# Optimization experiments

Hardware: AMD Instinct MI355X
Metric: run time of the kernel (lower is better)

The kernel has to match this reference:

```python
import jax, jax.numpy as jnp
import numpy as np

K = 1024      # num_embeddings
D = 256       # embedding_dim
BETA = 0.25


def setup_inputs() -> dict:
    key = jax.random.key(0)
    k1, k2 = jax.random.split(key)
    z = jax.random.normal(k1, (4, D, 16, 32, 32), dtype=jnp.float32)
    # matches torch init: uniform(-1/K, 1/K)
    embedding = jax.random.uniform(k2, (K, D), dtype=jnp.float32,
                                   minval=-1.0 / K, maxval=1.0 / K)
    return {"z": z, "embedding": embedding}


def reference(z, embedding):
    # z: (B, C, Dd, H, W) with C == D
    z_perm = jnp.transpose(z, (0, 2, 3, 4, 1))          # (B, Dd, H, W, C)
    flat = z_perm.reshape(-1, D)                        # (N, D)

    dist = (jnp.sum(flat * flat, axis=1, keepdims=True)
            + jnp.sum(embedding * embedding, axis=1)
            - 2.0 * flat @ embedding.T)
    indices_flat = jnp.argmin(dist, axis=1)             # (N,)

    # one-hot @ embedding == direct gather
    z_q_flat = embedding[indices_flat]                  # (N, D)
    z_q = z_q_flat.reshape(z_perm.shape)

    commitment_loss = jnp.mean((z_perm - jax.lax.stop_gradient(z_q)) ** 2)
    vq_loss = BETA * commitment_loss

    # straight-through estimator
    z_q_st = z_perm + jax.lax.stop_gradient(z_q - z_perm)
    z_q_out = jnp.transpose(z_q_st, (0, 4, 1, 2, 3))    # back to (B, C, Dd, H, W)

    # perplexity from assignment histogram
    n = flat.shape[0]
    counts = jnp.zeros((K,), dtype=flat.dtype).at[indices_flat].add(1.0)
    avg_probs = counts / n
    perplexity = jnp.exp(-jnp.sum(avg_probs * jnp.log(avg_probs + 1e-10)))

    indices = indices_flat.reshape(z_perm.shape[:-1])   # (B, Dd, H, W)
    return z_q_out, vq_loss, indices, perplexity
```

## Files before the change

### kernel.cpp

```cpp
#include <hip/hip_runtime.h>

#define Dd 256
#define Kc 1024
#define SPATIAL 16384
#define NROWS 65536
#define NELEM 16777216
#define LOSS_OFF 16777216
#define IDX_OFF  16777217
#define PERP_OFF (16777217 + 65536)
#define MARGIN 3.5e-4f
#define RH_ROWS 8

typedef _Float16 f16x8 __attribute__((ext_vector_type(8)));
typedef float f32x4 __attribute__((ext_vector_type(4)));


__global__ __launch_bounds__(256) void prep2_kernel(const float* __restrict__ emb,
                                                    _Float16* __restrict__ efp,
                                                    float* __restrict__ eT,
                                                    float* __restrict__ se) {
  const int j = blockIdx.x, c = threadIdx.x;
  float v = emb[j * Dd + c];
  const int ct2 = j >> 4, l15 = j & 15;
  const int kk = c >> 5, q = (c >> 3) & 3, e = c & 7;
  efp[((size_t)(ct2 * 8 + kk) * 64 + q * 16 + l15) * 8 + e] = (_Float16)(v * 1024.0f);
  eT[c * Kc + j] = v;
  double s = (double)v * (double)v;
  #pragma unroll
  for (int off = 32; off; off >>= 1) s += __shfl_down(s, off, 64);
  __shared__ double ws4[4];
  if ((threadIdx.x & 63) == 0) ws4[threadIdx.x >> 6] = s;
  __syncthreads();
  if (threadIdx.x == 0) se[j] = (float)(ws4[0] + ws4[1] + ws4[2] + ws4[3]);
}

__global__ __launch_bounds__(512, 2) void prefilter2_kernel(const float* __restrict__ z,
                                                            const _Float16* __restrict__ efp,
                                                            const float* __restrict__ se,
                                                            float* __restrict__ sx,
                                                            float* __restrict__ out_idx_f,
                                                            int* __restrict__ idx_i,
                                                            int* __restrict__ counts,
                                                            int* __restrict__ hardcnt,
                                                            int* __restrict__ hardlist,
                                                            double* __restrict__ loss_sum) {
  __shared__ _Float16 As[32 * 272];
  __shared__ float sxp[16][32];
  __shared__ float selds[Kc];
  __shared__ float rm1w[8][32];
  __shared__ float rm2w[8][32];
  __shared__ int   rc1w[8][32];

  const int tid = threadIdx.x;
  const int n0 = blockIdx.x * 32;
  const int b = n0 >> 14, s0 = n0 & 16383;
  const float* zb = z + (size_t)b * (Dd * SPATIAL) + s0;

  {
    const int r = tid & 31, cp = tid >> 5;
    float acc = 0.0f;
    #pragma unroll
    for (int c = cp * 16; c < cp * 16 + 16; ++c) {
      const float v = zb[(size_t)c * SPATIAL + r];
      As[r * 272 + c] = (_Float16)v;
      acc = fmaf(v, v, acc);
    }
    sxp[cp][r] = acc;
  }
  selds[tid] = se[tid];
  selds[tid + 512] = se[tid + 512];
  __syncthreads();

  float sxv = 0.0f;
  if (tid < 32) {
    float s = 0.0f;
    #pragma unroll
    for (int p = 0; p < 16; ++p) s += sxp[p][tid];
    sxv = s;
    sx[n0 + tid] = s;
  }

  const int w = tid >> 6, lane = tid & 63, q = lane >> 4, l15 = lane & 15;
  const int colbase = w * 128;

  f16x8 Afrag[2][8];
  #pragma unroll
  for (int rt = 0; rt < 2; ++rt)
    #pragma unroll
    for (int kk = 0; kk < 8; ++kk)
      Afrag[rt][kk] = *(const f16x8*)(&As[(rt * 16 + l15) * 272 + kk * 32 + q * 8]);

  float m1[8], m2[8];
  int   c1[8];
  #pragma unroll
  for (int i = 0; i < 8; ++i) { m1[i] = 3.4e38f; m2[i] = 3.4e38f; c1[i] = 0; }

  #pragma unroll
  for (int ct = 0; ct < 8; ++ct) {
    const _Float16* bp = efp + ((size_t)((w * 8 + ct) * 8) * 64 + lane) * 8;
    f32x4 a0 = {0.f, 0.f, 0.f, 0.f}, a1 = {0.f, 0.f, 0.f, 0.f};
    #pragma unroll
    for (int kk = 0; kk < 8; ++kk) {
      const f16x8 B = *(const f16x8*)(bp + kk * 512);
      a0 = __builtin_amdgcn_mfma_f32_16x16x32_f16(Afrag[0][kk], B, a0, 0, 0, 0);
      a1 = __builtin_amdgcn_mfma_f32_16x16x32_f16(Afrag[1][kk], B, a1, 0, 0, 0);
    }
    const int col = colbase + ct * 16 + l15;
    const float sec = selds[col];
    #pragma unroll
    for (int reg = 0; reg < 4; ++reg) {
      const float sc0 = fmaf(-0.001953125f, a0[reg], sec);
      const float sc1 = fmaf(-0.001953125f, a1[reg], sec);
      m2[reg] = fminf(m2[reg], fmaxf(m1[reg], sc0));
      c1[reg] = (sc0 < m1[reg]) ? col : c1[reg];
      m1[reg] = fminf(m1[reg], sc0);
      m2[4 + reg] = fminf(m2[4 + reg], fmaxf(m1[4 + reg], sc1));
      c1[4 + reg] = (sc1 < m1[4 + reg]) ? col : c1[4 + reg];
      m1[4 + reg] = fminf(m1[4 + reg], sc1);
    }
  }

  #pragma unroll
  for (int m = 1; m <= 8; m <<= 1) {
    #pragma unroll
    for (int i = 0; i < 8; ++i) {
      const float om1 = __shfl_xor(m1[i], m, 64);
      const float om2 = __shfl_xor(m2[i], m, 64);
      const int   oc1 = __shfl_xor(c1[i], m, 64);
      m2[i] = fminf(fminf(m2[i], om2), fmaxf(m1[i], om1));
      if (om1 < m1[i]) { m1[i] = om1; c1[i] = oc1; }
    }
  }
  if (l15 == 0) {
    #pragma unroll
    for (int reg = 0; reg < 4; ++reg) {
      rm1w[w][q * 4 + reg] = m1[reg];
      rm2w[w][q * 4 + reg] = m2[reg];
      rc1w[w][q * 4 + reg] = c1[reg];
      rm1w[w][16 + q * 4 + reg] = m1[4 + reg];
      rm2w[w][16 + q * 4 + reg] = m2[4 + reg];
      rc1w[w][16 + q * 4 + reg] = c1[4 + reg];
    }
  }
  __syncthreads();

  if (tid < 64) {
    double lp = 0.0;
    int hard = 0;
    const int n = n0 + tid;
    if (tid < 32) {
      float bm1 = rm1w[0][tid], bm2 = rm2w[0][tid];
      int   bc1 = rc1w[0][tid];
      #pragma unroll
      for (int ww = 1; ww < 8; ++ww) {
        const float a1v = rm1w[ww][tid], a2v = rm2w[ww][tid];
        const int   ac = rc1w[ww][tid];
        bm2 = fminf(fminf(bm2, a2v), fmaxf(bm1, a1v));
        if (a1v < bm1) { bm1 = a1v; bc1 = ac; }
      }
      if (bm2 >= bm1 + MARGIN) {
        idx_i[n] = bc1;
        out_idx_f[n] = (float)bc1;
        atomicAdd(&counts[bc1], 1);
        lp = (double)sxv + (double)bm1;
      } else {
        hard = 1;
      }
    }
    const unsigned long long mask = __ballot(hard);
    const int h = __popcll(mask);
    int base = 0;
    if (tid == 0 && h) base = atomicAdd(hardcnt, h);
    base = __shfl(base, 0, 64);
    if (hard) {
      const int rank = __popcll(mask & ((1ull << tid) - 1ull));
      hardlist[base + rank] = n;
    }
    #pragma unroll
    for (int off = 32; off; off >>= 1) lp += __shfl_down(lp, off, 64);
    if (tid == 0 && lp != 0.0) atomicAdd(loss_sum, lp);
  }
}

__global__ __launch_bounds__(256) void resolve_hard_kernel(const float* __restrict__ z,
                                                           const float* __restrict__ eT,
                                                           const float* __restrict__ se,
                                                           const float* __restrict__ sx,
                                                           const int* __restrict__ hardcnt,
                                                           const int* __restrict__ hardlist,
                                                           float* __restrict__ out_idx_f,
                                                           int* __restrict__ idx_i,
                                                           int* __restrict__ counts,
                                                           double* __restrict__ loss_sum) {
  const int hc = *hardcnt;
  const int i0 = blockIdx.x * RH_ROWS;
  if (i0 >= hc) return;
  const int tid = threadIdx.x;

  __shared__ int   sn[RH_ROWS];
  __shared__ float sxs[RH_ROWS];
  __shared__ __align__(16) float zxT[Dd][12];
  __shared__ float redS[RH_ROWS][4];
  __shared__ int   redI[RH_ROWS][4];
  __shared__ double dred[RH_ROWS];

  if (tid < RH_ROWS) {
    const int ii = i0 + tid;
    const int n = (ii < hc) ? hardlist[ii] : hardlist[i0];
    sn[tid] = n;
    sxs[tid] = sx[n];
  }
  __syncthreads();

  {
    const int r = tid >> 5, cs = tid & 31;
    const int n = sn[r], b = n >> 14, s = n & 16383;
    const float* zr = z + (size_t)b * (Dd * SPATIAL) + s;
    #pragma unroll
    for (int k = 0; k < 8; ++k)
      zxT[cs + 32 * k][r] = zr[(size_t)(cs + 32 * k) * SPATIAL];
  }
  __syncthreads();

  const int w = tid >> 6, lane = tid & 63;
  const int jbase = w * 256 + 4 * lane;
  const float4 se4v = *(const float4*)(se + jbase);
  const float ses4[4] = {se4v.x, se4v.y, se4v.z, se4v.w};

  float acc[RH_ROWS][4];
  #pragma unroll
  for (int r = 0; r < RH_ROWS; ++r)
    #pragma unroll
    for (int cc = 0; cc < 4; ++cc) acc[r][cc] = 0.f;

  const float* ecol = eT + jbase;
  #pragma unroll 4
  for (int c = 0; c < Dd; ++c) {
    const float4 bv = *(const float4*)(ecol + (size_t)c * Kc);
    const float4 a0 = *(const float4*)(&zxT[c][0]);
    const float4 a1 = *(const float4*)(&zxT[c][4]);
    const float za[8] = {a0.x, a0.y, a0.z, a0.w, a1.x, a1.y, a1.z, a1.w};
    #pragma unroll
    for (int r = 0; r < RH_ROWS; ++r) {
      acc[r][0] = fmaf(za[r], bv.x, acc[r][0]);
      acc[r][1] = fmaf(za[r], bv.y, acc[r][1]);
      acc[r][2] = fmaf(za[r], bv.z, acc[r][2]);
      acc[r][3] = fmaf(za[r], bv.w, acc[r][3]);
    }
  }

  #pragma unroll
  for (int r = 0; r < RH_ROWS; ++r) {
    const float sxr = sxs[r];
    float s1 = 3.4e38f;
    int   j1 = 0x7fffffff;
    #pragma unroll
    for (int cc = 0; cc < 4; ++cc) {
      const int j = jbase + cc;
      const float t1 = sxr + ses4[cc];
      const float sv = t1 - 2.0f * acc[r][cc];
      if (sv < s1 || (sv == s1 && j < j1)) { s1 = sv; j1 = j; }
    }
    #pragma unroll
    for (int m = 1; m <= 32; m <<= 1) {
      const float so = __shfl_xor(s1, m, 64);
      const int   jo = __shfl_xor(j1, m, 64);
      if (so < s1 || (so == s1 && jo < j1)) { s1 = so; j1 = jo; }
    }
    if (lane == 0) { redS[r][w] = s1; redI[r][w] = j1; }
  }
  __syncthreads();

  if (tid < RH_ROWS) {
    float bs = redS[tid][0];
    int   bj = redI[tid][0];
    #pragma unroll
    for (int ww = 1; ww < 4; ++ww) {
      const float a1 = redS[tid][ww];
      const int   aj = redI[tid][ww];
      if (a1 < bs || (a1 == bs && aj < bj)) { bs = a1; bj = aj; }
    }
    double lp = 0.0;
    if (i0 + tid < hc) {
      const int n = sn[tid];
      idx_i[n] = bj;
      out_idx_f[n] = (float)bj;
      atomicAdd(&counts[bj], 1);
      lp = (double)bs;
    }
    dred[tid] = lp;
  }
  __syncthreads();
  if (tid == 0) {
    double t = 0.0;
    #pragma unroll
    for (int r = 0; r < RH_ROWS; ++r) t += dred[r];
    if (t != 0.0) atomicAdd(loss_sum, t);
  }
}

__global__ __launch_bounds__(256) void phase2c_kernel(const float* __restrict__ emb,
                                                      const int* __restrict__ idx_i,
                                                      float* __restrict__ out_zq) {
  __shared__ float els[64 * 257];
  __shared__ int sidx[64];
  const int tid = threadIdx.x;
  const int blk = blockIdx.x, b = blk >> 8, s0 = (blk & 255) << 6;
  if (tid < 64) sidx[tid] = idx_i[b * SPATIAL + s0 + tid];
  __syncthreads();
  {
    const int rr = tid >> 2, p = tid & 3;
    const float* ep = emb + (size_t)sidx[rr] * Dd + p * 64;
    float* dl = els + rr * 257 + p * 64;
    #pragma unroll
    for (int i = 0; i < 64; i += 4) {
      const float4 e4 = *(const float4*)(ep + i);
      dl[i] = e4.x; dl[i + 1] = e4.y; dl[i + 2] = e4.z; dl[i + 3] = e4.w;
    }
  }
  __syncthreads();
  const int s4 = tid & 15, cg = tid >> 4;
  const size_t zb = (size_t)b * (Dd * SPATIAL);
  #pragma unroll 4
  for (int c = cg; c < Dd; c += 16) {
    float4 v;
    v.x = els[(s4 * 4 + 0) * 257 + c];
    v.y = els[(s4 * 4 + 1) * 257 + c];
    v.z = els[(s4 * 4 + 2) * 257 + c];
    v.w = els[(s4 * 4 + 3) * 257 + c];
    *(float4*)(out_zq + zb + (size_t)c * SPATIAL + s0 + s4 * 4) = v;
  }
}

__global__ __launch_bounds__(256) void finalize_kernel(const int* __restrict__ counts,
                                                       const double* __restrict__ loss_sum,
                                                       float* __restrict__ out) {
  const int tid = threadIdx.x;
  double local = 0.0;
  for (int k = tid; k < Kc; k += 256) {
    const double p = (double)counts[k] / (double)NROWS;
    local += p * log(p + 1e-10);
  }
  #pragma unroll
  for (int off = 32; off; off >>= 1) local += __shfl_down(local, off, 64);
  __shared__ double dred[4];
  if ((tid & 63) == 0) dred[tid >> 6] = local;
  __syncthreads();
  if (tid == 0) {
    const double H = dred[0] + dred[1] + dred[2] + dred[3];
    out[PERP_OFF] = (float)exp(-H);
    out[LOSS_OFF] = (float)(0.25 * loss_sum[0] / (double)NELEM);
  }
}


__global__ __launch_bounds__(256) void prep_kernel(const float* __restrict__ emb,
                                                   float* __restrict__ eT,
                                                   float* __restrict__ se) {
  const int j = blockIdx.x, c = threadIdx.x;
  float v = emb[j * Dd + c];
  eT[c * Kc + j] = v;
  double s = (double)v * (double)v;
  #pragma unroll
  for (int off = 32; off; off >>= 1) s += __shfl_down(s, off, 64);
  __shared__ double ws4[4];
  if ((threadIdx.x & 63) == 0) ws4[threadIdx.x >> 6] = s;
  __syncthreads();
  if (threadIdx.x == 0) se[j] = (float)(ws4[0] + ws4[1] + ws4[2] + ws4[3]);
}

__global__ __launch_bounds__(256) void sx_kernel(const float* __restrict__ z,
                                                 float* __restrict__ sx) {
  __shared__ double part[4][64];
  const int tid = threadIdx.x, r = tid & 63, cg = tid >> 6;
  const int blk = blockIdx.x, b = blk >> 8, s0 = (blk & 255) << 6;
  const float* zb = z + (size_t)b * (Dd * SPATIAL);
  double acc = 0.0;
  for (int c = cg * 64; c < cg * 64 + 64; ++c) {
    const float v = zb[(size_t)c * SPATIAL + s0 + r];
    acc += (double)v * (double)v;
  }
  part[cg][r] = acc;
  __syncthreads();
  if (tid < 64)
    sx[b * SPATIAL + s0 + tid] =
        (float)(part[0][tid] + part[1][tid] + part[2][tid] + part[3][tid]);
}

__global__ __launch_bounds__(256) void argmin_kernel(const float* __restrict__ z,
                                                     const float* __restrict__ eT,
                                                     const float* __restrict__ se,
                                                     const float* __restrict__ sx,
                                                     float* __restrict__ out_idx_f,
                                                     int* __restrict__ idx_i,
                                                     int* __restrict__ counts) {
  __shared__ float As[32 * 64];
  __shared__ float Bs[32 * 64];
  __shared__ float ses[Kc];
  __shared__ float sxs[64];
  __shared__ float redS1[64 * 16];
  __shared__ int   redI1[64 * 16];
  const int tid = threadIdx.x, tc = tid & 15, tr = tid >> 4;
  const int blk = blockIdx.x, b = blk >> 8, s0 = (blk & 255) << 6;
  const float* zb = z + (size_t)b * (Dd * SPATIAL);
  #pragma unroll
  for (int i = 0; i < 4; ++i) ses[tid + 256 * i] = se[tid + 256 * i];
  if (tid < 64) sxs[tid] = sx[b * SPATIAL + s0 + tid];
  float s1[4]; int j1[4];
  #pragma unroll
  for (int r = 0; r < 4; ++r) { s1[r] = 3.4e38f; j1[r] = 0; }
  for (int j0 = 0; j0 < Kc; j0 += 64) {
    float acc[4][4];
    #pragma unroll
    for (int rr = 0; rr < 4; ++rr)
      #pragma unroll
      for (int cc = 0; cc < 4; ++cc) acc[rr][cc] = 0.0f;
    for (int c0 = 0; c0 < Dd; c0 += 32) {
      __syncthreads();
      #pragma unroll
      for (int i = 0; i < 8; ++i) {
        const int e = i * 256 + tid, ci = e >> 6, r = e & 63;
        As[e] = zb[(size_t)(c0 + ci) * SPATIAL + s0 + r];
        Bs[e] = eT[(c0 + ci) * Kc + j0 + r];
      }
      __syncthreads();
      #pragma unroll
      for (int d = 0; d < 32; ++d) {
        const float4 av = *reinterpret_cast<const float4*>(&As[d * 64 + 4 * tr]);
        const float4 bv = *reinterpret_cast<const float4*>(&Bs[d * 64 + 4 * tc]);
        const float aa[4] = {av.x, av.y, av.z, av.w};
        const float bb[4] = {bv.x, bv.y, bv.z, bv.w};
        #pragma unroll
        for (int rr = 0; rr < 4; ++rr)
          #pragma unroll
          for (int cc = 0; cc < 4; ++cc)
            acc[rr][cc] = fmaf(aa[rr], bb[cc], acc[rr][cc]);
      }
    }
    #pragma unroll
    for (int rr = 0; rr < 4; ++rr) {
      const float sxr = sxs[4 * tr + rr];
      #pragma unroll
      for (int cc = 0; cc < 4; ++cc) {
        const int j = j0 + 4 * tc + cc;
        const float t1 = sxr + ses[j];
        const float s = t1 - 2.0f * acc[rr][cc];
        if (s < s1[rr] || (s == s1[rr] && j < j1[rr])) { s1[rr] = s; j1[rr] = j; }
      }
    }
  }
  #pragma unroll
  for (int rr = 0; rr < 4; ++rr) {
    redS1[(4 * tr + rr) * 16 + tc] = s1[rr];
    redI1[(4 * tr + rr) * 16 + tc] = j1[rr];
  }
  __syncthreads();
  if (tid < 64) {
    float bs = redS1[tid * 16];
    int bj = redI1[tid * 16];
    #pragma unroll
    for (int t = 1; t < 16; ++t) {
      const float a1 = redS1[tid * 16 + t];
      const int aj = redI1[tid * 16 + t];
      if (a1 < bs || (a1 == bs && aj < bj)) { bs = a1; bj = aj; }
    }
    const int n = b * SPATIAL + s0 + tid;
    out_idx_f[n] = (float)bj;
    idx_i[n] = bj;
    atomicAdd(&counts[bj], 1);
  }
}

__global__ __launch_bounds__(256) void phase2_kernel(const float* __restrict__ z,
                                                     const float* __restrict__ eT,
                                                     const int* __restrict__ idx_i,
                                                     float* __restrict__ out_zq,
                                                     double* __restrict__ loss_sum) {
  __shared__ int sidx[64];
  __shared__ double dred[4];
  const int tid = threadIdx.x;
  const int blk = blockIdx.x, b = blk >> 8, s0 = (blk & 255) << 6;
  if (tid < 64) sidx[tid] = idx_i[b * SPATIAL + s0 + tid];
  __syncthreads();
  const int s = tid & 63, coff = tid >> 6;
  const size_t zb = (size_t)b * (Dd * SPATIAL);
  const int myidx = sidx[s];
  double lsum = 0.0;
  for (int c = coff; c < Dd; c += 4) {
    const size_t off = zb + (size_t)c * SPATIAL + s0 + s;
    const float zv = z[off];
    const float zq = eT[c * Kc + myidx];
    out_zq[off] = zv + (zq - zv);
    const float d = zv - zq;
    lsum += (double)d * (double)d;
  }
  #pragma unroll
  for (int off = 32; off; off >>= 1) lsum += __shfl_down(lsum, off, 64);
  if ((tid & 63) == 0) dred[tid >> 6] = lsum;
  __syncthreads();
  if (tid == 0) atomicAdd(loss_sum, dred[0] + dred[1] + dred[2] + dred[3]);
}


extern "C" void kernel_launch(void* const* d_in, const int* in_sizes, int n_in,
                              void* d_out, int out_size, void* d_ws, size_t ws_size,
                              hipStream_t stream) {
  const float* z   = (const float*)d_in[0];
  const float* emb = (const float*)d_in[1];
  float* out = (float*)d_out;
  char* ws = (char*)d_ws;

  const size_t OFF_SE   = 8192;
  const size_t OFF_SX   = 12288;
  const size_t OFF_EF   = 274432;
  const size_t OFF_IDX  = 1060864;
  const size_t OFF_ET   = 1585152;
  const size_t OFF_HARD = 3682304;
  const size_t NEED     = 3944448;

  double* loss_sum = (double*)(ws + 0);
  int*    hardcnt  = (int*)(ws + 8);
  int*    counts   = (int*)(ws + 256);

  hipMemsetAsync(d_ws, 0, 8192, stream);

  if (ws_size >= NEED) {
    float*    se        = (float*)(ws + OFF_SE);
    float*    sx        = (float*)(ws + OFF_SX);
    _Float16* efp       = (_Float16*)(ws + OFF_EF);
    int*      idx_i     = (int*)(ws + OFF_IDX);
    float*    eT        = (float*)(ws + OFF_ET);
    int*      hardlist  = (int*)(ws + OFF_HARD);

    prep2_kernel<<<Kc, 256, 0, stream>>>(emb, efp, eT, se);
    prefilter2_kernel<<<2048, 512, 0, stream>>>(z, efp, se, sx,
                                                out + IDX_OFF, idx_i, counts,
                                                hardcnt, hardlist, loss_sum);
    resolve_hard_kernel<<<NROWS / RH_ROWS, 256, 0, stream>>>(
        z, eT, se, sx, hardcnt, hardlist, out + IDX_OFF, idx_i, counts, loss_sum);
    phase2c_kernel<<<1024, 256, 0, stream>>>(emb, idx_i, out);
    finalize_kernel<<<1, 256, 0, stream>>>(counts, loss_sum, out);
  } else {
    float* eT    = (float*)(ws + 8192);
    float* se    = (float*)(ws + 8192 + 1048576);
    float* sx    = (float*)(ws + 8192 + 1048576 + 4096);
    int*   idx_i = (int*)(ws + 8192 + 1048576 + 4096 + 262144);

    prep_kernel<<<Kc, 256, 0, stream>>>(emb, eT, se);
    sx_kernel<<<1024, 256, 0, stream>>>(z, sx);
    argmin_kernel<<<1024, 256, 0, stream>>>(z, eT, se, sx, out + IDX_OFF, idx_i, counts);
    phase2_kernel<<<1024, 256, 0, stream>>>(z, eT, idx_i, out, loss_sum);
    finalize_kernel<<<1, 256, 0, stream>>>(counts, loss_sum, out);
  }
}
```

Baseline: 287.0 us.

## Retile prefilter to 64 rows per block with 4 waves and B-fragment reuse

```diff
diff --git a/kernel.cpp b/kernel.cpp
--- a/kernel.cpp
+++ b/kernel.cpp
@@ -10,6 +10,7 @@
 #define PERP_OFF (16777217 + 65536)
 #define MARGIN 3.5e-4f
 #define RH_ROWS 8
+#define ASTRIDE 264
 
 typedef _Float16 f16x8 __attribute__((ext_vector_type(8)));
 typedef float f32x4 __attribute__((ext_vector_type(4)));
@@ -34,96 +35,89 @@
   if (threadIdx.x == 0) se[j] = (float)(ws4[0] + ws4[1] + ws4[2] + ws4[3]);
 }
 
-__global__ __launch_bounds__(512, 2) void prefilter2_kernel(const float* __restrict__ z,
-                                                            const _Float16* __restrict__ efp,
-                                                            const float* __restrict__ se,
-                                                            float* __restrict__ sx,
-                                                            float* __restrict__ out_idx_f,
-                                                            int* __restrict__ idx_i,
-                                                            int* __restrict__ counts,
-                                                            int* __restrict__ hardcnt,
-                                                            int* __restrict__ hardlist,
-                                                            double* __restrict__ loss_sum) {
-  __shared__ _Float16 As[32 * 272];
-  __shared__ float sxp[16][32];
+__global__ __launch_bounds__(256) void prefilter2_kernel(const float* __restrict__ z,
+                                                         const _Float16* __restrict__ efp,
+                                                         const float* __restrict__ se,
+                                                         float* __restrict__ sx,
+                                                         float* __restrict__ out_idx_f,
+                                                         int* __restrict__ idx_i,
+                                                         int* __restrict__ counts,
+                                                         int* __restrict__ hardcnt,
+                                                         int* __restrict__ hardlist,
+                                                         double* __restrict__ loss_sum) {
+  __shared__ _Float16 As[64 * ASTRIDE];
+  __shared__ float sxp[4][64];
   __shared__ float selds[Kc];
-  __shared__ float rm1w[8][32];
-  __shared__ float rm2w[8][32];
-  __shared__ int   rc1w[8][32];
+  __shared__ float rm1w[4][64];
+  __shared__ float rm2w[4][64];
+  __shared__ int   rc1w[4][64];
 
   const int tid = threadIdx.x;
-  const int n0 = blockIdx.x * 32;
+  const int n0 = blockIdx.x * 64;
   const int b = n0 >> 14, s0 = n0 & 16383;
   const float* zb = z + (size_t)b * (Dd * SPATIAL) + s0;
 
   {
-    const int r = tid & 31, cp = tid >> 5;
+    const int r = tid & 63, cp = tid >> 6;
     float acc = 0.0f;
     #pragma unroll
-    for (int c = cp * 16; c < cp * 16 + 16; ++c) {
+    for (int c = cp * 64; c < cp * 64 + 64; ++c) {
       const float v = zb[(size_t)c * SPATIAL + r];
-      As[r * 272 + c] = (_Float16)v;
+      As[r * ASTRIDE + c] = (_Float16)v;
       acc = fmaf(v, v, acc);
     }
     sxp[cp][r] = acc;
   }
-  selds[tid] = se[tid];
-  selds[tid + 512] = se[tid + 512];
+  #pragma unroll
+  for (int i = 0; i < 4; ++i) selds[tid + 256 * i] = se[tid + 256 * i];
   __syncthreads();
 
   float sxv = 0.0f;
-  if (tid < 32) {
-    float s = 0.0f;
-    #pragma unroll
-    for (int p = 0; p < 16; ++p) s += sxp[p][tid];
+  if (tid < 64) {
+    float s = sxp[0][tid] + sxp[1][tid] + sxp[2][tid] + sxp[3][tid];
     sxv = s;
     sx[n0 + tid] = s;
   }
 
   const int w = tid >> 6, lane = tid & 63, q = lane >> 4, l15 = lane & 15;
-  const int colbase = w * 128;
-
-  f16x8 Afrag[2][8];
-  #pragma unroll
-  for (int rt = 0; rt < 2; ++rt)
-    #pragma unroll
-    for (int kk = 0; kk < 8; ++kk)
-      Afrag[rt][kk] = *(const f16x8*)(&As[(rt * 16 + l15) * 272 + kk * 32 + q * 8]);
-
-  float m1[8], m2[8];
-  int   c1[8];
-  #pragma unroll
-  for (int i = 0; i < 8; ++i) { m1[i] = 3.4e38f; m2[i] = 3.4e38f; c1[i] = 0; }
-
-  #pragma unroll
-  for (int ct = 0; ct < 8; ++ct) {
-    const _Float16* bp = efp + ((size_t)((w * 8 + ct) * 8) * 64 + lane) * 8;
-    f32x4 a0 = {0.f, 0.f, 0.f, 0.f}, a1 = {0.f, 0.f, 0.f, 0.f};
-    #pragma unroll
-    for (int kk = 0; kk < 8; ++kk) {
-      const f16x8 B = *(const f16x8*)(bp + kk * 512);
-      a0 = __builtin_amdgcn_mfma_f32_16x16x32_f16(Afrag[0][kk], B, a0, 0, 0, 0);
-      a1 = __builtin_amdgcn_mfma_f32_16x16x32_f16(Afrag[1][kk], B, a1, 0, 0, 0);
-    }
+  const int colbase = w * 256;
+
+  float m1[16], m2[16];
+  int   c1[16];
+  #pragma unroll
+  for (int i = 0; i < 16; ++i) { m1[i] = 3.4e38f; m2[i] = 3.4e38f; c1[i] = 0; }
+
+  #pragma unroll 2
+  for (int ct = 0; ct < 16; ++ct) {
+    const _Float16* bp = efp + ((size_t)((w * 16 + ct) * 8) * 64 + lane) * 8;
+    f16x8 B[8];
+    #pragma unroll
+    for (int kk = 0; kk < 8; ++kk) B[kk] = *(const f16x8*)(bp + kk * 512);
     const int col = colbase + ct * 16 + l15;
     const float sec = selds[col];
     #pragma unroll
-    for (int reg = 0; reg < 4; ++reg) {
-      const float sc0 = fmaf(-0.001953125f, a0[reg], sec);
-      const float sc1 = fmaf(-0.001953125f, a1[reg], sec);
-      m2[reg] = fminf(m2[reg], fmaxf(m1[reg], sc0));
-      c1[reg] = (sc0 < m1[reg]) ? col : c1[reg];
-      m1[reg] = fminf(m1[reg], sc0);
-      m2[4 + reg] = fminf(m2[4 + reg], fmaxf(m1[4 + reg], sc1));
-      c1[4 + reg] = (sc1 < m1[4 + reg]) ? col : c1[4 + reg];
-      m1[4 + reg] = fminf(m1[4 + reg], sc1);
+    for (int rt = 0; rt < 4; ++rt) {
+      f32x4 a = {0.f, 0.f, 0.f, 0.f};
+      #pragma unroll
+      for (int kk = 0; kk < 8; ++kk) {
+        const f16x8 A = *(const f16x8*)(&As[(rt * 16 + l15) * ASTRIDE + kk * 32 + q * 8]);
+        a = __builtin_amdgcn_mfma_f32_16x16x32_f16(A, B[kk], a, 0, 0, 0);
+      }
+      #pragma unroll
+      for (int reg = 0; reg < 4; ++reg) {
+        const float sc = fmaf(-0.001953125f, a[reg], sec);
+        const int sl = rt * 4 + reg;
+        m2[sl] = fminf(m2[sl], fmaxf(m1[sl], sc));
+        c1[sl] = (sc < m1[sl]) ? col : c1[sl];
+        m1[sl] = fminf(m1[sl], sc);
+      }
     }
   }
 
   #pragma unroll
   for (int m = 1; m <= 8; m <<= 1) {
     #pragma unroll
-    for (int i = 0; i < 8; ++i) {
+    for (int i = 0; i < 16; ++i) {
       const float om1 = __shfl_xor(m1[i], m, 64);
       const float om2 = __shfl_xor(m2[i], m, 64);
       const int   oc1 = __shfl_xor(c1[i], m, 64);
@@ -133,14 +127,14 @@
   }
   if (l15 == 0) {
     #pragma unroll
-    for (int reg = 0; reg < 4; ++reg) {
-      rm1w[w][q * 4 + reg] = m1[reg];
-      rm2w[w][q * 4 + reg] = m2[reg];
-      rc1w[w][q * 4 + reg] = c1[reg];
-      rm1w[w][16 + q * 4 + reg] = m1[4 + reg];
-      rm2w[w][16 + q * 4 + reg] = m2[4 + reg];
-      rc1w[w][16 + q * 4 + reg] = c1[4 + reg];
-    }
+    for (int rt = 0; rt < 4; ++rt)
+      #pragma unroll
+      for (int reg = 0; reg < 4; ++reg) {
+        const int row = rt * 16 + q * 4 + reg;
+        rm1w[w][row] = m1[rt * 4 + reg];
+        rm2w[w][row] = m2[rt * 4 + reg];
+        rc1w[w][row] = c1[rt * 4 + reg];
+      }
   }
   __syncthreads();
 
@@ -148,11 +142,11 @@
     double lp = 0.0;
     int hard = 0;
     const int n = n0 + tid;
-    if (tid < 32) {
+    {
       float bm1 = rm1w[0][tid], bm2 = rm2w[0][tid];
       int   bc1 = rc1w[0][tid];
       #pragma unroll
-      for (int ww = 1; ww < 8; ++ww) {
+      for (int ww = 1; ww < 4; ++ww) {
         const float a1v = rm1w[ww][tid], a2v = rm2w[ww][tid];
         const int   ac = rc1w[ww][tid];
         bm2 = fminf(fminf(bm2, a2v), fmaxf(bm1, a1v));
@@ -533,9 +527,9 @@
     int*      hardlist  = (int*)(ws + OFF_HARD);
 
     prep2_kernel<<<Kc, 256, 0, stream>>>(emb, efp, eT, se);
-    prefilter2_kernel<<<2048, 512, 0, stream>>>(z, efp, se, sx,
-                                                out + IDX_OFF, idx_i, counts,
-                                                hardcnt, hardlist, loss_sum);
+    prefilter2_kernel<<<NROWS / 64, 256, 0, stream>>>(z, efp, se, sx,
+                                                      out + IDX_OFF, idx_i, counts,
+                                                      hardcnt, hardlist, loss_sum);
     resolve_hard_kernel<<<NROWS / RH_ROWS, 256, 0, stream>>>(
         z, eT, se, sx, hardcnt, hardlist, out + IDX_OFF, idx_i, counts, loss_sum);
     phase2c_kernel<<<1024, 256, 0, stream>>>(emb, idx_i, out);
```

After: 266.7 us. -7.1%, faster.
